# Kernel tuning notes

Measured on AMD Instinct MI355X. Metric: run time of the kernel, lower is better.

The kernel has to match this reference:

```python
import jax, jax.numpy as jnp
import numpy as np

EPS = 1e-8


def _cdist(a, b):
    # a: [B,N,3], b: [B,M,3] -> euclidean distances [B,N,M]
    a2 = jnp.sum(a * a, axis=-1)[:, :, None]          # [B,N,1]
    b2 = jnp.sum(b * b, axis=-1)[:, None, :]          # [B,1,M]
    ab = jnp.einsum('bnd,bmd->bnm', a, b)             # [B,N,M]
    d2 = jnp.maximum(a2 + b2 - 2.0 * ab, 0.0)
    return jnp.sqrt(d2)


def setup_inputs() -> dict:
    key = jax.random.key(0)
    ks = jax.random.split(key, 8)
    B, N, M, C1, C2 = 16, 4096, 1024, 128, 256
    Cin = C1 + C2  # 384
    H1, H2 = 256, 128
    return {
        'xyz1': jax.random.normal(ks[0], (B, N, 3), dtype=jnp.float32),
        'xyz2': jax.random.normal(ks[1], (B, M, 3), dtype=jnp.float32),
        'points1': jax.random.normal(ks[2], (B, C1, N), dtype=jnp.float32),
        'points2': jax.random.normal(ks[3], (B, C2, M), dtype=jnp.float32),
        'W1': jax.random.normal(ks[4], (H1, Cin), dtype=jnp.float32) * (1.0 / np.sqrt(Cin)),
        'b1': jnp.zeros((H1,), dtype=jnp.float32),
        'W2': jax.random.normal(ks[5], (H2, H1), dtype=jnp.float32) * (1.0 / np.sqrt(H1)),
        'b2': jnp.zeros((H2,), dtype=jnp.float32),
    }


def reference(xyz1, xyz2, points1, points2, W1, b1, W2, b2):
    # inverse-distance weighted interpolation over ALL M source points
    dist = _cdist(xyz1, xyz2) + EPS                   # [B,N,M]
    inv = 1.0 / dist
    weight = inv / jnp.sum(inv, axis=-1, keepdims=True)
    # interpolated features: [B,N,M] @ [B,M,C2] -> [B,C2,N]
    interpolated = jnp.einsum('bnm,bcm->bcn', weight, points2)
    new_points = jnp.concatenate([points1, interpolated], axis=1)  # [B,C1+C2,N]
    # 1x1 Conv1d MLP with ReLU
    h = jax.nn.relu(jnp.einsum('oc,bcn->bon', W1, new_points) + b1[None, :, None])
    out = jax.nn.relu(jnp.einsum('oc,bcn->bon', W2, h) + b2[None, :, None])
    return out
```

## Files before the change

kernel.cpp:

```cpp
#include <hip/hip_runtime.h>
#include <math.h>

#define BBATCH 16
#define NPTS   4096
#define MPTS   1024
#define C1c    128
#define C2c    256
#define CINc   384
#define H1c    256
#define H2c    128
#define TN     64

typedef _Float16 f16x8 __attribute__((ext_vector_type(8)));
typedef _Float16 f16x4 __attribute__((ext_vector_type(4)));
typedef float    f32x4 __attribute__((ext_vector_type(4)));

#define BAR() do { asm volatile("s_waitcnt lgkmcnt(0)" ::: "memory"); \
                   __builtin_amdgcn_s_barrier(); } while (0)

#define INV_HALF   8192
#define OFF_XYZ2   32768
#define OFF_RED    49152
#define SMEM_BYTES 51200

#define NFRAG_P2  (BBATCH * 32 * 16 * 64)
#define NFRAG_W1  (16 * 12 * 64)
#define NFRAG_W2  (8 * 8 * 64)
#define WS_P2S  0
#define WS_W1S  (NFRAG_P2 * 8)
#define WS_W2S  (WS_W1S + NFRAG_W1 * 8)
#define WS_F16_TOTAL (WS_W2S + NFRAG_W2 * 8)

__global__ __launch_bounds__(256) void cvt_swz(
    const float* __restrict__ p2, const float* __restrict__ W1,
    const float* __restrict__ W2, _Float16* __restrict__ ws)
{
    const int t = blockIdx.x * 256 + threadIdx.x;
    const float* src;
    _Float16* dst;
    if (t < NFRAG_P2) {
        const int lane = t & 63, wt = (t >> 6) & 15, s = (t >> 10) & 31, b = t >> 15;
        const int c = wt * 16 + (lane & 15);
        const int m = s * 32 + (lane >> 4) * 8;
        src = p2 + ((size_t)(b * C2c + c)) * MPTS + m;
        dst = ws + WS_P2S + (size_t)t * 8;
    } else if (t < NFRAG_P2 + NFRAG_W1) {
        const int u = t - NFRAG_P2;
        const int lane = u & 63, kc = (u >> 6) % 12, wt = (u >> 6) / 12;
        const int o = wt * 16 + (lane & 15);
        const int k = kc * 32 + (lane >> 4) * 8;
        src = W1 + (size_t)o * CINc + k;
        dst = ws + WS_W1S + (size_t)u * 8;
    } else {
        const int v = t - NFRAG_P2 - NFRAG_W1;
        const int lane = v & 63, oc = (v >> 6) & 7, wt2 = v >> 9;
        const int o = wt2 * 16 + (lane & 15);
        const int k = oc * 32 + (lane >> 4) * 8;
        src = W2 + (size_t)o * H1c + k;
        dst = ws + WS_W2S + (size_t)v * 8;
    }
    const float4 a0 = *(const float4*)(src);
    const float4 a1 = *(const float4*)(src + 4);
    f16x8 h;
    h[0] = (_Float16)a0.x; h[1] = (_Float16)a0.y; h[2] = (_Float16)a0.z; h[3] = (_Float16)a0.w;
    h[4] = (_Float16)a1.x; h[5] = (_Float16)a1.y; h[6] = (_Float16)a1.z; h[7] = (_Float16)a1.w;
    *(f16x8*)dst = h;
}

template <bool F16P>
__global__ __launch_bounds__(512, 8) void fp_mfma14(
    const float* __restrict__ xyz1, const float* __restrict__ xyz2,
    const float* __restrict__ p1,   const float* __restrict__ p2,
    const float* __restrict__ W1,   const float* __restrict__ b1v,
    const float* __restrict__ W2,   const float* __restrict__ b2v,
    const _Float16* __restrict__ p2s, const _Float16* __restrict__ W1s,
    const _Float16* __restrict__ W2s,
    float* __restrict__ out)
{
    __shared__ __align__(16) char smem[SMEM_BYTES];
    _Float16* s_inv  = (_Float16*)smem;
    _Float16* s_X    = (_Float16*)smem;
    _Float16* s_H    = (_Float16*)smem;
    float*    s_xyz2 = (float*)(smem + OFF_XYZ2);
    float*    s_red  = (float*)(smem + OFF_RED);

    const int tid  = threadIdx.x;
    const int w    = tid >> 6;
    const int L    = tid & 63;
    const int quad = L >> 4;
    const int l16  = L & 15;

    const int id = blockIdx.x;
    const int b  = (id & 7) * 2 + ((id >> 3) & 1);
    const int n0 = (id >> 4) * TN;

    const float* __restrict__ z2b = xyz2 + (size_t)b * MPTS * 3;
    const float* __restrict__ p2b = p2   + (size_t)b * C2c * MPTS;
    const _Float16* __restrict__ p2sb =
        F16P ? (p2s + (((size_t)b * 32 * 16 + (size_t)w * 2) * 64 + L) * 8) : (const _Float16*)nullptr;

    for (int i = tid; i < MPTS * 3 / 4; i += 512)
        ((f32x4*)s_xyz2)[i] = ((const f32x4*)z2b)[i];

    const float x1x = xyz1[((size_t)b * NPTS + n0 + L) * 3 + 0];
    const float x1y = xyz1[((size_t)b * NPTS + n0 + L) * 3 + 1];
    const float x1z = xyz1[((size_t)b * NPTS + n0 + L) * 3 + 2];

    f32x4 acc[2][4];
    #pragma unroll
    for (int ct = 0; ct < 2; ++ct)
        #pragma unroll
        for (int nt = 0; nt < 4; ++nt)
            acc[ct][nt] = (f32x4){0.f, 0.f, 0.f, 0.f};

    float ssum = 0.f;
    f16x8 Aa[4][2];

    auto loadA = [&](int s, f16x8 dst[2]) {
        if (F16P) {
            const _Float16* ap = p2sb + (size_t)s * (16 * 64 * 8);
            #pragma unroll
            for (int ct = 0; ct < 2; ++ct)
                dst[ct] = *(const f16x8*)(ap + (size_t)ct * (64 * 8));
        } else {
            const float* ap = p2b + (size_t)(w * 32 + l16) * MPTS + s * 32 + quad * 8;
            #pragma unroll
            for (int ct = 0; ct < 2; ++ct) {
                const float4 a0 = *(const float4*)(ap + (size_t)ct * (16 * MPTS));
                const float4 a1 = *(const float4*)(ap + (size_t)ct * (16 * MPTS) + 4);
                f16x8 h;
                h[0] = (_Float16)a0.x; h[1] = (_Float16)a0.y; h[2] = (_Float16)a0.z; h[3] = (_Float16)a0.w;
                h[4] = (_Float16)a1.x; h[5] = (_Float16)a1.y; h[6] = (_Float16)a1.z; h[7] = (_Float16)a1.w;
                dst[ct] = h;
            }
        }
    };

    auto gen_g = [&](int ss_, int g) {
        _Float16* buf = s_inv + (ss_ & 1) * INV_HALF;
        const float* zp = s_xyz2 + (size_t)(ss_ * 128 + w * 16 + g * 8) * 3;
        f32x4 zr[6];
        #pragma unroll
        for (int j = 0; j < 6; ++j) zr[j] = ((const f32x4*)zp)[j];
        const float* zv = (const float*)zr;
        f16x8 iv;
        #pragma unroll
        for (int i = 0; i < 8; ++i) {
            const float dx = x1x - zv[3 * i + 0];
            const float dy = x1y - zv[3 * i + 1];
            const float dz = x1z - zv[3 * i + 2];
            const float d2 = fmaf(dx, dx, fmaf(dy, dy, fmaf(dz, dz, 1e-12f)));
            const float inv = __builtin_amdgcn_rsqf(d2);
            ssum += inv;
            iv[i] = (_Float16)inv;
        }
        *(f16x8*)(buf + ((((w >> 1) * 4 + quad) * 64) + ((w & 1) * 2 + g) * 16 + l16) * 8) = iv;
    };

    loadA(0, Aa[0]);
    loadA(1, Aa[1]);
    BAR();
    gen_g(0, 0);
    gen_g(0, 1);
    BAR();

    for (int ss = 0; ss < 7; ++ss) {
        const _Float16* buf = s_inv + (ss & 1) * INV_HALF;
        #pragma unroll
        for (int cc = 0; cc < 4; ++cc) {
            const int s = ss * 4 + cc;
            loadA(s + 2, Aa[(cc + 2) & 3]);
            if (cc < 2) gen_g(ss + 1, cc);
            __builtin_amdgcn_s_setprio(1);
            #pragma unroll
            for (int nt = 0; nt < 4; ++nt) {
                const f16x8 bf = *(const f16x8*)(buf + ((cc * 4 + nt) * 64 + L) * 8);
                #pragma unroll
                for (int ct = 0; ct < 2; ++ct)
                    acc[ct][nt] = __builtin_amdgcn_mfma_f32_16x16x32_f16(Aa[cc][ct], bf, acc[ct][nt], 0, 0, 0);
            }
            __builtin_amdgcn_s_setprio(0);
        }
        BAR();
    }

    float tv[2][8];
    {
        #pragma unroll
        for (int h = 0; h < 2; ++h) {
            const int f  = w * 2 + h;
            const int kq = f >> 2, nt = f & 3;
            const float* pp = p1 + ((size_t)b * C1c + kq * 32 + quad * 8) * NPTS + n0 + nt * 16 + l16;
            #pragma unroll
            for (int j = 0; j < 8; ++j) tv[h][j] = pp[(size_t)j * NPTS];
        }
    }
    {
        const _Float16* buf = s_inv + INV_HALF;
        #pragma unroll
        for (int cc = 0; cc < 4; ++cc) {
            if (cc < 2) loadA(28 + cc + 2, Aa[(cc + 2) & 3]);
            __builtin_amdgcn_s_setprio(1);
            #pragma unroll
            for (int nt = 0; nt < 4; ++nt) {
                const f16x8 bf = *(const f16x8*)(buf + ((cc * 4 + nt) * 64 + L) * 8);
                #pragma unroll
                for (int ct = 0; ct < 2; ++ct)
                    acc[ct][nt] = __builtin_amdgcn_mfma_f32_16x16x32_f16(Aa[cc][ct], bf, acc[ct][nt], 0, 0, 0);
            }
            __builtin_amdgcn_s_setprio(0);
        }
    }
    {
        #pragma unroll
        for (int h = 0; h < 2; ++h) {
            const int f = w * 2 + h;
            f16x8 v;
            #pragma unroll
            for (int j = 0; j < 8; ++j) v[j] = (_Float16)tv[h][j];
            *(f16x8*)(s_X + ((size_t)f * 64 + L) * 8) = v;
        }
    }
    s_red[tid] = ssum;
    BAR();

    if (tid < 64) {
        float s = 0.f;
        #pragma unroll
        for (int wv = 0; wv < 8; ++wv) s += s_red[wv * 64 + tid];
        s_red[tid] = 1.0f / s;
    }
    BAR();

    f16x8 afP[2][2];
    auto loadW1 = [&](int kc, f16x8 dst[2]) {
        if (F16P) {
            const _Float16* wp = W1s + (((size_t)(w * 2) * 12 + kc) * 64 + L) * 8;
            #pragma unroll
            for (int ct = 0; ct < 2; ++ct)
                dst[ct] = *(const f16x8*)(wp + (size_t)ct * (12 * 64 * 8));
        } else {
            const float* wp = W1 + (size_t)(w * 32 + l16) * CINc + kc * 32 + quad * 8;
            #pragma unroll
            for (int ct = 0; ct < 2; ++ct) {
                const float4 a0 = *(const float4*)(wp + ct * (16 * CINc));
                const float4 a1 = *(const float4*)(wp + ct * (16 * CINc) + 4);
                f16x8 h;
                h[0] = (_Float16)a0.x; h[1] = (_Float16)a0.y; h[2] = (_Float16)a0.z; h[3] = (_Float16)a0.w;
                h[4] = (_Float16)a1.x; h[5] = (_Float16)a1.y; h[6] = (_Float16)a1.z; h[7] = (_Float16)a1.w;
                dst[ct] = h;
            }
        }
    };
    loadW1(0, afP[0]);

    {
        float rn4[4];
        #pragma unroll
        for (int nt = 0; nt < 4; ++nt) rn4[nt] = s_red[nt * 16 + l16];
        #pragma unroll
        for (int ct = 0; ct < 2; ++ct) {
            const int kq = 4 + w;
            const int lp = (ct * 2 + (quad >> 1)) * 16 + l16;
            const int jo = (quad & 1) * 4;
            #pragma unroll
            for (int nt = 0; nt < 4; ++nt) {
                const f32x4 v = acc[ct][nt];
                const float r = rn4[nt];
                f16x4 hv;
                hv[0] = (_Float16)(v[0] * r);
                hv[1] = (_Float16)(v[1] * r);
                hv[2] = (_Float16)(v[2] * r);
                hv[3] = (_Float16)(v[3] * r);
                *(f16x4*)(s_X + (((size_t)(kq * 4 + nt)) * 64 + lp) * 8 + jo) = hv;
            }
        }
    }
    BAR();

    f32x4 hacc[2][4];
    #pragma unroll
    for (int ct = 0; ct < 2; ++ct)
        #pragma unroll
        for (int nt = 0; nt < 4; ++nt)
            hacc[ct][nt] = (f32x4){0.f, 0.f, 0.f, 0.f};

    #pragma unroll
    for (int kc = 0; kc < 12; ++kc) {
        if (kc + 1 < 12) loadW1(kc + 1, afP[(kc + 1) & 1]);
        __builtin_amdgcn_s_setprio(1);
        #pragma unroll
        for (int nt = 0; nt < 4; ++nt) {
            const f16x8 bf = *(const f16x8*)(s_X + (((size_t)(kc * 4 + nt)) * 64 + L) * 8);
            #pragma unroll
            for (int ct = 0; ct < 2; ++ct)
                hacc[ct][nt] = __builtin_amdgcn_mfma_f32_16x16x32_f16(afP[kc & 1][ct], bf, hacc[ct][nt], 0, 0, 0);
        }
        __builtin_amdgcn_s_setprio(0);
    }

    BAR();

    f16x8 afP2[2];
    auto loadW2 = [&](int oc, f16x8& dst) {
        if (F16P) {
            dst = *(const f16x8*)(W2s + (((size_t)(w * 8 + oc)) * 64 + L) * 8);
        } else {
            const float* wp = W2 + (size_t)(w * 16 + l16) * H1c + oc * 32 + quad * 8;
            const float4 a0 = *(const float4*)(wp);
            const float4 a1 = *(const float4*)(wp + 4);
            f16x8 h;
            h[0] = (_Float16)a0.x; h[1] = (_Float16)a0.y; h[2] = (_Float16)a0.z; h[3] = (_Float16)a0.w;
            h[4] = (_Float16)a1.x; h[5] = (_Float16)a1.y; h[6] = (_Float16)a1.z; h[7] = (_Float16)a1.w;
            dst = h;
        }
    };
    loadW2(0, afP2[0]);

    {
        f32x4 bb[2];
        #pragma unroll
        for (int ct = 0; ct < 2; ++ct)
            bb[ct] = *(const f32x4*)(b1v + w * 32 + ct * 16 + quad * 4);
        #pragma unroll
        for (int ct = 0; ct < 2; ++ct) {
            const int lp = (ct * 2 + (quad >> 1)) * 16 + l16;
            const int jo = (quad & 1) * 4;
            #pragma unroll
            for (int nt = 0; nt < 4; ++nt) {
                const f32x4 v = hacc[ct][nt];
                f16x4 hv;
                hv[0] = (_Float16)fmaxf(v[0] + bb[ct][0], 0.f);
                hv[1] = (_Float16)fmaxf(v[1] + bb[ct][1], 0.f);
                hv[2] = (_Float16)fmaxf(v[2] + bb[ct][2], 0.f);
                hv[3] = (_Float16)fmaxf(v[3] + bb[ct][3], 0.f);
                *(f16x4*)(s_H + (((size_t)(w * 4 + nt)) * 64 + lp) * 8 + jo) = hv;
            }
        }
    }
    BAR();

    f32x4 oacc[4];
    #pragma unroll
    for (int nt = 0; nt < 4; ++nt)
        oacc[nt] = (f32x4){0.f, 0.f, 0.f, 0.f};

    #pragma unroll
    for (int oc = 0; oc < 8; ++oc) {
        if (oc + 1 < 8) loadW2(oc + 1, afP2[(oc + 1) & 1]);
        __builtin_amdgcn_s_setprio(1);
        #pragma unroll
        for (int nt = 0; nt < 4; ++nt) {
            const f16x8 bf = *(const f16x8*)(s_H + (((size_t)(oc * 4 + nt)) * 64 + L) * 8);
            oacc[nt] = __builtin_amdgcn_mfma_f32_16x16x32_f16(afP2[oc & 1], bf, oacc[nt], 0, 0, 0);
        }
        __builtin_amdgcn_s_setprio(0);
    }

    {
        const f32x4 bb2 = *(const f32x4*)(b2v + w * 16 + quad * 4);
        #pragma unroll
        for (int nt = 0; nt < 4; ++nt) {
            float* op = out + ((size_t)b * H2c + w * 16 + quad * 4) * NPTS
                            + n0 + nt * 16 + l16;
            #pragma unroll
            for (int j = 0; j < 4; ++j)
                op[(size_t)j * NPTS] = fmaxf(oacc[nt][j] + bb2[j], 0.f);
        }
    }
}

extern "C" void kernel_launch(void* const* d_in, const int* in_sizes, int n_in,
                              void* d_out, int out_size, void* d_ws, size_t ws_size,
                              hipStream_t stream) {
    (void)in_sizes; (void)n_in; (void)out_size;
    const float* xyz1 = (const float*)d_in[0];
    const float* xyz2 = (const float*)d_in[1];
    const float* p1   = (const float*)d_in[2];
    const float* p2   = (const float*)d_in[3];
    const float* W1   = (const float*)d_in[4];
    const float* b1   = (const float*)d_in[5];
    const float* W2   = (const float*)d_in[6];
    const float* b2   = (const float*)d_in[7];
    float* out = (float*)d_out;

    dim3 grid(BBATCH * (NPTS / TN));
    dim3 block(512);
    if (ws_size >= (size_t)WS_F16_TOTAL * 2) {
        _Float16* ws = (_Float16*)d_ws;
        const int nswz = NFRAG_P2 + NFRAG_W1 + NFRAG_W2;
        cvt_swz<<<dim3(nswz / 256), dim3(256), 0, stream>>>(p2, W1, W2, ws);
        fp_mfma14<true><<<grid, block, 0, stream>>>(xyz1, xyz2, p1, p2, W1, b1, W2, b2,
                                                    ws + WS_P2S, ws + WS_W1S, ws + WS_W2S, out);
    } else {
        fp_mfma14<false><<<grid, block, 0, stream>>>(xyz1, xyz2, p1, p2, W1, b1, W2, b2,
                                                     nullptr, nullptr, nullptr, out);
    }
}
```

Baseline: 160.1 us.

## Halve inverse-distance LDS buffers and read points1 directly in first MLP layer

Measured after the change: 507.7 us. 217% more time.

```diff
diff --git a/kernel.cpp b/kernel.cpp
--- a/kernel.cpp
+++ b/kernel.cpp
@@ -18,10 +18,10 @@
 #define BAR() do { asm volatile("s_waitcnt lgkmcnt(0)" ::: "memory"); \
                    __builtin_amdgcn_s_barrier(); } while (0)
 
-#define INV_HALF   8192
-#define OFF_XYZ2   32768
-#define OFF_RED    49152
-#define SMEM_BYTES 51200
+#define INV_HALF   4096
+#define OFF_XYZ2   16384
+#define OFF_RED    32768
+#define SMEM_BYTES 34816
 
 #define NFRAG_P2  (BBATCH * 32 * 16 * 64)
 #define NFRAG_W1  (16 * 12 * 64)
@@ -68,7 +68,7 @@
 }
 
 template <bool F16P>
-__global__ __launch_bounds__(512, 8) void fp_mfma14(
+__global__ __launch_bounds__(512, 8) void fp_mfma15(
     const float* __restrict__ xyz1, const float* __restrict__ xyz2,
     const float* __restrict__ p1,   const float* __restrict__ p2,
     const float* __restrict__ W1,   const float* __restrict__ b1v,
@@ -136,9 +136,9 @@
         }
     };
 
-    auto gen_g = [&](int ss_, int g) {
+    auto gen = [&](int ss_) {
         _Float16* buf = s_inv + (ss_ & 1) * INV_HALF;
-        const float* zp = s_xyz2 + (size_t)(ss_ * 128 + w * 16 + g * 8) * 3;
+        const float* zp = s_xyz2 + (size_t)(ss_ * 64 + w * 8) * 3;
         f32x4 zr[6];
         #pragma unroll
         for (int j = 0; j < 6; ++j) zr[j] = ((const f32x4*)zp)[j];
@@ -154,76 +154,45 @@
             ssum += inv;
             iv[i] = (_Float16)inv;
         }
-        *(f16x8*)(buf + ((((w >> 1) * 4 + quad) * 64) + ((w & 1) * 2 + g) * 16 + l16) * 8) = iv;
+        *(f16x8*)(buf + ((((w >> 2) * 4 + (L >> 4)) * 64) + (w & 3) * 16 + l16) * 8) = iv;
+    };
+
+    auto mmac = [&](const _Float16* buf, int cc, f16x8 A_[2]) {
+        __builtin_amdgcn_s_setprio(1);
+        #pragma unroll
+        for (int nt = 0; nt < 4; ++nt) {
+            const f16x8 bf = *(const f16x8*)(buf + ((cc * 4 + nt) * 64 + L) * 8);
+            #pragma unroll
+            for (int ct = 0; ct < 2; ++ct)
+                acc[ct][nt] = __builtin_amdgcn_mfma_f32_16x16x32_f16(A_[ct], bf, acc[ct][nt], 0, 0, 0);
+        }
+        __builtin_amdgcn_s_setprio(0);
     };
 
     loadA(0, Aa[0]);
     loadA(1, Aa[1]);
     BAR();
-    gen_g(0, 0);
-    gen_g(0, 1);
-    BAR();
-
-    for (int ss = 0; ss < 7; ++ss) {
-        const _Float16* buf = s_inv + (ss & 1) * INV_HALF;
-        #pragma unroll
-        for (int cc = 0; cc < 4; ++cc) {
-            const int s = ss * 4 + cc;
-            loadA(s + 2, Aa[(cc + 2) & 3]);
-            if (cc < 2) gen_g(ss + 1, cc);
-            __builtin_amdgcn_s_setprio(1);
-            #pragma unroll
-            for (int nt = 0; nt < 4; ++nt) {
-                const f16x8 bf = *(const f16x8*)(buf + ((cc * 4 + nt) * 64 + L) * 8);
-                #pragma unroll
-                for (int ct = 0; ct < 2; ++ct)
-                    acc[ct][nt] = __builtin_amdgcn_mfma_f32_16x16x32_f16(Aa[cc][ct], bf, acc[ct][nt], 0, 0, 0);
-            }
-            __builtin_amdgcn_s_setprio(0);
-        }
+    gen(0);
+    BAR();
+
+    for (int sp = 0; sp < 8; ++sp) {
+        const int s4 = sp * 4;
+        if (s4 + 2 < 32) loadA(s4 + 2, Aa[2]);
+        gen(2 * sp + 1);
+        mmac(s_inv, 0, Aa[0]);
+        if (s4 + 3 < 32) loadA(s4 + 3, Aa[3]);
+        mmac(s_inv, 1, Aa[1]);
         BAR();
-    }
-
-    float tv[2][8];
-    {
-        #pragma unroll
-        for (int h = 0; h < 2; ++h) {
-            const int f  = w * 2 + h;
-            const int kq = f >> 2, nt = f & 3;
-            const float* pp = p1 + ((size_t)b * C1c + kq * 32 + quad * 8) * NPTS + n0 + nt * 16 + l16;
-            #pragma unroll
-            for (int j = 0; j < 8; ++j) tv[h][j] = pp[(size_t)j * NPTS];
-        }
-    }
-    {
-        const _Float16* buf = s_inv + INV_HALF;
-        #pragma unroll
-        for (int cc = 0; cc < 4; ++cc) {
-            if (cc < 2) loadA(28 + cc + 2, Aa[(cc + 2) & 3]);
-            __builtin_amdgcn_s_setprio(1);
-            #pragma unroll
-            for (int nt = 0; nt < 4; ++nt) {
-                const f16x8 bf = *(const f16x8*)(buf + ((cc * 4 + nt) * 64 + L) * 8);
-                #pragma unroll
-                for (int ct = 0; ct < 2; ++ct)
-                    acc[ct][nt] = __builtin_amdgcn_mfma_f32_16x16x32_f16(Aa[cc][ct], bf, acc[ct][nt], 0, 0, 0);
-            }
-            __builtin_amdgcn_s_setprio(0);
-        }
-    }
-    {
-        #pragma unroll
-        for (int h = 0; h < 2; ++h) {
-            const int f = w * 2 + h;
-            f16x8 v;
-            #pragma unroll
-            for (int j = 0; j < 8; ++j) v[j] = (_Float16)tv[h][j];
-            *(f16x8*)(s_X + ((size_t)f * 64 + L) * 8) = v;
-        }
-    }
+        if (s4 + 4 < 32) loadA(s4 + 4, Aa[0]);
+        if (2 * sp + 2 < 16) gen(2 * sp + 2);
+        mmac(s_inv + INV_HALF, 0, Aa[2]);
+        if (s4 + 5 < 32) loadA(s4 + 5, Aa[1]);
+        mmac(s_inv + INV_HALF, 1, Aa[3]);
+        BAR();
+    }
+
     s_red[tid] = ssum;
     BAR();
-
     if (tid < 64) {
         float s = 0.f;
         #pragma unroll
@@ -260,7 +229,6 @@
         for (int nt = 0; nt < 4; ++nt) rn4[nt] = s_red[nt * 16 + l16];
         #pragma unroll
         for (int ct = 0; ct < 2; ++ct) {
-            const int kq = 4 + w;
             const int lp = (ct * 2 + (quad >> 1)) * 16 + l16;
             const int jo = (quad & 1) * 4;
             #pragma unroll
@@ -272,7 +240,7 @@
                 hv[1] = (_Float16)(v[1] * r);
                 hv[2] = (_Float16)(v[2] * r);
                 hv[3] = (_Float16)(v[3] * r);
-                *(f16x4*)(s_X + (((size_t)(kq * 4 + nt)) * 64 + lp) * 8 + jo) = hv;
+                *(f16x4*)(s_X + (((size_t)(w * 4 + nt)) * 64 + lp) * 8 + jo) = hv;
             }
         }
     }
@@ -285,13 +253,24 @@
         for (int nt = 0; nt < 4; ++nt)
             hacc[ct][nt] = (f32x4){0.f, 0.f, 0.f, 0.f};
 
+    const float* p1base = p1 + (size_t)b * C1c * NPTS + n0;
     #pragma unroll
     for (int kc = 0; kc < 12; ++kc) {
         if (kc + 1 < 12) loadW1(kc + 1, afP[(kc + 1) & 1]);
         __builtin_amdgcn_s_setprio(1);
         #pragma unroll
         for (int nt = 0; nt < 4; ++nt) {
-            const f16x8 bf = *(const f16x8*)(s_X + (((size_t)(kc * 4 + nt)) * 64 + L) * 8);
+            f16x8 bf;
+            if (kc < 4) {
+                const float* pp = p1base + (size_t)(kc * 32 + quad * 8) * NPTS + nt * 16 + l16;
+                float t[8];
+                #pragma unroll
+                for (int j = 0; j < 8; ++j) t[j] = pp[(size_t)j * NPTS];
+                #pragma unroll
+                for (int j = 0; j < 8; ++j) bf[j] = (_Float16)t[j];
+            } else {
+                bf = *(const f16x8*)(s_X + (((size_t)((kc - 4) * 4 + nt)) * 64 + L) * 8);
+            }
             #pragma unroll
             for (int ct = 0; ct < 2; ++ct)
                 hacc[ct][nt] = __builtin_amdgcn_mfma_f32_16x16x32_f16(afP[kc & 1][ct], bf, hacc[ct][nt], 0, 0, 0);
@@ -390,10 +369,10 @@
         _Float16* ws = (_Float16*)d_ws;
         const int nswz = NFRAG_P2 + NFRAG_W1 + NFRAG_W2;
         cvt_swz<<<dim3(nswz / 256), dim3(256), 0, stream>>>(p2, W1, W2, ws);
-        fp_mfma14<true><<<grid, block, 0, stream>>>(xyz1, xyz2, p1, p2, W1, b1, W2, b2,
+        fp_mfma15<true><<<grid, block, 0, stream>>>(xyz1, xyz2, p1, p2, W1, b1, W2, b2,
                                                     ws + WS_P2S, ws + WS_W1S, ws + WS_W2S, out);
     } else {
-        fp_mfma14<false><<<grid, block, 0, stream>>>(xyz1, xyz2, p1, p2, W1, b1, W2, b2,
+        fp_mfma15<false><<<grid, block, 0, stream>>>(xyz1, xyz2, p1, p2, W1, b1, W2, b2,
                                                      nullptr, nullptr, nullptr, out);
     }
 }
```
